# Optimization experiments

Measured on AMD Instinct MI355X. Metric: run time of the kernel, lower is better.

The kernel has to match this reference:

```python
import jax, jax.numpy as jnp
import numpy as np

N_NODES = 100000
N_EDGES = 1600000
IN_FEATS = 256
OUT_FEATS = 128


def setup_inputs() -> dict:
    key = jax.random.key(0)
    k1, k2, k3, k4 = jax.random.split(key, 4)
    feat = jax.random.normal(k1, (N_NODES, IN_FEATS), dtype=jnp.float32)
    # Glorot-uniform-like weight
    limit = np.sqrt(6.0 / (IN_FEATS + OUT_FEATS)).astype(np.float32)
    weight = jax.random.uniform(k2, (IN_FEATS, OUT_FEATS), dtype=jnp.float32,
                                minval=-limit, maxval=limit)
    bias = jnp.zeros((OUT_FEATS,), dtype=jnp.float32)
    src = jax.random.randint(k3, (N_EDGES,), 0, N_NODES, dtype=jnp.int32)
    dst = jax.random.randint(k4, (N_EDGES,), 0, N_NODES, dtype=jnp.int32)
    return {"feat": feat, "weight": weight, "bias": bias, "src": src, "dst": dst}


def reference(feat, weight, bias, src, dst):
    n = feat.shape[0]
    # in-degree per node (edges point src -> dst), clipped to >= 1
    deg = jax.ops.segment_sum(jnp.ones_like(dst, dtype=feat.dtype), dst,
                              num_segments=n)
    norm = jnp.clip(deg, 1.0, None) ** -0.5          # [N]
    norm = norm[:, None]                             # [N, 1]
    h = feat * norm                                  # src-side normalization
    # in_feats > out_feats: project first, then aggregate (cheaper messages)
    h = h @ weight                                   # [N, out]
    agg = jax.ops.segment_sum(h[src], dst, num_segments=n)  # sparse sum-aggregate
    rst = agg * norm + bias                          # dst-side norm + bias
    return rst
```

## Files before the change

kernel.cpp:

```cpp
#include <hip/hip_runtime.h>

#define IN_F 256
#define OUT_F 128
#define BSH 7
#define BNODES 128
#define MAXBUCK 1024
#define BIN_BLOCKS 256

typedef short bf16x8 __attribute__((ext_vector_type(8)));
typedef float f32x4 __attribute__((ext_vector_type(4)));

__device__ inline unsigned short f2bf(float x) {
    union { float f; unsigned u; } v; v.f = x;
    unsigned r = v.u + 0x7FFFu + ((v.u >> 16) & 1u);
    return (unsigned short)(r >> 16);
}
__device__ inline float bf2f(unsigned short x) {
    union { unsigned u; float f; } v; v.u = ((unsigned)x) << 16;
    return v.f;
}

__global__ __launch_bounds__(256) void wprep_kernel(const float* __restrict__ W,
                                                    unsigned short* __restrict__ Wt,
                                                    int* __restrict__ bhist) {
    int n = blockIdx.x;
    int k = threadIdx.x;
    Wt[n * IN_F + k] = f2bf(W[k * OUT_F + n]);
    if (threadIdx.x < 8) bhist[blockIdx.x * 8 + threadIdx.x] = 0;
}

__global__ __launch_bounds__(256) void bin1a_kernel(const int* __restrict__ dst,
                                                    int* __restrict__ bhist,
                                                    int n_edges, int nbuck) {
    __shared__ int hist[MAXBUCK];
    const int tid = threadIdx.x;
    const int chunk = (n_edges + gridDim.x - 1) / gridDim.x;
    const int lo = blockIdx.x * chunk;
    const int hi = min(lo + chunk, n_edges);

    for (int i = tid; i < MAXBUCK; i += 256) hist[i] = 0;
    __syncthreads();
    for (int e = lo + tid; e < hi; e += 256)
        atomicAdd(&hist[dst[e] >> BSH], 1);
    __syncthreads();
    for (int i = tid; i < nbuck; i += 256) {
        int c = hist[i];
        if (c) atomicAdd(&bhist[i], c);
    }
}

__global__ __launch_bounds__(1024) void scanb_kernel(const int* __restrict__ bhist,
                                                     int* __restrict__ bstart,
                                                     int* __restrict__ gcur,
                                                     int* __restrict__ rstart,
                                                     int nbuck, int n_nodes) {
    __shared__ int sh[1024];
    int tid = threadIdx.x;
    int v = (tid < nbuck) ? bhist[tid] : 0;
    sh[tid] = v;
    __syncthreads();
    #pragma unroll
    for (int off = 1; off < 1024; off <<= 1) {
        int t = (tid >= off) ? sh[tid - off] : 0;
        __syncthreads();
        sh[tid] += t;
        __syncthreads();
    }
    int ex = sh[tid] - v;
    if (tid < nbuck) { bstart[tid] = ex; gcur[tid] = ex; }
    if (tid == 1023) {
        bstart[nbuck] = sh[1023];
        rstart[n_nodes] = sh[1023];
    }
}

__global__ __launch_bounds__(256) void bin1b_kernel(const int* __restrict__ src,
                                                    const int* __restrict__ dst,
                                                    int* __restrict__ gcur,
                                                    unsigned* __restrict__ ebuf,
                                                    int n_edges, int nbuck) {
    __shared__ int hist[MAXBUCK];
    __shared__ int lbase[MAXBUCK];
    const int tid = threadIdx.x;
    const int chunk = (n_edges + gridDim.x - 1) / gridDim.x;
    const int lo = blockIdx.x * chunk;
    const int hi = min(lo + chunk, n_edges);

    for (int i = tid; i < nbuck; i += 256) hist[i] = 0;
    __syncthreads();
    for (int e = lo + tid; e < hi; e += 256)
        atomicAdd(&hist[dst[e] >> BSH], 1);
    __syncthreads();
    for (int i = tid; i < nbuck; i += 256) {
        int c = hist[i];
        lbase[i] = (c > 0) ? atomicAdd(&gcur[i], c) : 0;
        hist[i] = 0;
    }
    __syncthreads();
    for (int e = lo + tid; e < hi; e += 256) {
        int d = dst[e];
        int bkt = d >> BSH;
        int off = atomicAdd(&hist[bkt], 1);
        ebuf[lbase[bkt] + off] = ((unsigned)src[e] << BSH) | (unsigned)(d & (BNODES - 1));
    }
}

__global__ __launch_bounds__(256) void bin2_kernel(const unsigned* __restrict__ ebuf,
                                                   const int* __restrict__ bstart,
                                                   int* __restrict__ rstart,
                                                   float* __restrict__ norm,
                                                   int* __restrict__ eidx,
                                                   int n_nodes) {
    __shared__ int lcnt[BNODES];
    __shared__ int lex[BNODES];
    const int tid = threadIdx.x;
    const int node0 = blockIdx.x << BSH;
    const int e0 = bstart[blockIdx.x];
    const int e1 = bstart[blockIdx.x + 1];

    if (tid < BNODES) lcnt[tid] = 0;
    __syncthreads();
    for (int e = e0 + tid; e < e1; e += 256)
        atomicAdd(&lcnt[ebuf[e] & (BNODES - 1)], 1);
    __syncthreads();

    int own = (tid < BNODES) ? lcnt[tid] : 0;
    if (tid < BNODES) lex[tid] = own;
    __syncthreads();
    #pragma unroll
    for (int off = 1; off < BNODES; off <<= 1) {
        int t = (tid >= off && tid < BNODES) ? lex[tid - off] : 0;
        __syncthreads();
        if (tid < BNODES) lex[tid] += t;
        __syncthreads();
    }
    if (tid < BNODES) {
        int ex = lex[tid] - own;
        lex[tid] = ex;
        int g = node0 + tid;
        if (g <= n_nodes) rstart[g] = e0 + ex;
        if (g < n_nodes) {
            float d = (float)own;
            if (d < 1.0f) d = 1.0f;
            norm[g] = 1.0f / sqrtf(d);
        }
        lcnt[tid] = 0;
    }
    __syncthreads();

    for (int e = e0 + tid; e < e1; e += 256) {
        unsigned pk = ebuf[e];
        int dl = pk & (BNODES - 1);
        int pos = atomicAdd(&lcnt[dl], 1);
        eidx[e0 + lex[dl] + pos] = (int)(pk >> BSH);
    }
}

__global__ __launch_bounds__(512) void gemm_mfma(const float* __restrict__ feat,
                                                 const unsigned short* __restrict__ Wt,
                                                 unsigned short* __restrict__ h,
                                                 int n_nodes) {
    __shared__ unsigned short Bs[OUT_F * IN_F];

    const int tid  = threadIdx.x;
    const int wave = tid >> 6;
    const int lane = tid & 63;
    const int r0   = (blockIdx.x * 8 + wave) * 16;
    const int lrow = lane & 15;
    const int g    = lane >> 4;
    const int kgrp = g * 8;

    {
        const f32x4* srcv = reinterpret_cast<const f32x4*>(Wt);
        f32x4* dstv = reinterpret_cast<f32x4*>(Bs);
        #pragma unroll
        for (int i = 0; i < 8; ++i) {
            int c   = tid + i * 512;
            int row = c >> 5;
            int col = c & 31;
            dstv[c] = srcv[row * 32 + (col ^ (row & 7))];
        }
    }

    const int row  = r0 + lrow;
    const int rowc = (row < n_nodes) ? row : (n_nodes - 1);
    const float* arow = feat + (size_t)rowc * IN_F;

    f32x4 a[16];
    #pragma unroll
    for (int k0 = 0; k0 < IN_F / 32; ++k0) {
        a[2 * k0]     = *reinterpret_cast<const f32x4*>(arow + k0 * 32 + kgrp);
        a[2 * k0 + 1] = *reinterpret_cast<const f32x4*>(arow + k0 * 32 + kgrp + 4);
    }
    #pragma unroll
    for (int i = 0; i < 16; ++i)
        asm volatile("" : "+v"(a[i]));

    __syncthreads();

    f32x4 acc[8];
    #pragma unroll
    for (int n = 0; n < 8; ++n) acc[n] = (f32x4){0.f, 0.f, 0.f, 0.f};

    const bf16x8* bsv = reinterpret_cast<const bf16x8*>(Bs);

    #pragma unroll
    for (int k0 = 0; k0 < IN_F / 32; ++k0) {
        const f32x4 a0 = a[2 * k0];
        const f32x4 a1 = a[2 * k0 + 1];
        bf16x8 afr;
        afr[0] = (short)f2bf(a0[0]);
        afr[1] = (short)f2bf(a0[1]);
        afr[2] = (short)f2bf(a0[2]);
        afr[3] = (short)f2bf(a0[3]);
        afr[4] = (short)f2bf(a1[0]);
        afr[5] = (short)f2bf(a1[1]);
        afr[6] = (short)f2bf(a1[2]);
        afr[7] = (short)f2bf(a1[3]);
        #pragma unroll
        for (int n = 0; n < 8; ++n) {
            const int brow = n * 16 + lrow;
            bf16x8 bfr = bsv[brow * 32 + ((k0 * 4 + g) ^ (brow & 7))];
            acc[n] = __builtin_amdgcn_mfma_f32_16x16x32_bf16(afr, bfr, acc[n], 0, 0, 0);
        }
    }

    const int orow0 = r0 + g * 4;
    #pragma unroll
    for (int n = 0; n < 8; ++n) {
        #pragma unroll
        for (int j = 0; j < 4; ++j) {
            int orow = orow0 + j;
            if (orow < n_nodes)
                h[(size_t)orow * OUT_F + n * 16 + lrow] = f2bf(acc[n][j]);
        }
    }
}

__global__ __launch_bounds__(256) void agg_kernel(const unsigned short* __restrict__ h,
                                                  const int* __restrict__ eidx,
                                                  const int* __restrict__ rstart,
                                                  const float* __restrict__ norm,
                                                  const float* __restrict__ bias,
                                                  float* __restrict__ out,
                                                  int n_nodes) {
    const int wave = threadIdx.x >> 6;
    const int lane = threadIdx.x & 63;
    const int node = blockIdx.x * 4 + wave;
    if (node >= n_nodes) return;

    const int start = rstart[node];
    const int cnt   = rstart[node + 1] - start;

    float a0 = 0.f, a1 = 0.f;
    for (int base = 0; base < cnt; base += 64) {
        const int rem = min(64, cnt - base);
        int   ev = (lane < rem) ? eidx[start + base + lane] : 0;
        float nv = (lane < rem) ? norm[ev] : 0.f;

        int j = 0;
        for (; j + 4 <= rem; j += 4) {
            int s0 = __shfl(ev, j),     s1 = __shfl(ev, j + 1);
            int s2 = __shfl(ev, j + 2), s3 = __shfl(ev, j + 3);
            float n0 = __shfl(nv, j),     n1 = __shfl(nv, j + 1);
            float n2 = __shfl(nv, j + 2), n3 = __shfl(nv, j + 3);
            unsigned v0 = *reinterpret_cast<const unsigned*>(h + (size_t)s0 * OUT_F + lane * 2);
            unsigned v1 = *reinterpret_cast<const unsigned*>(h + (size_t)s1 * OUT_F + lane * 2);
            unsigned v2 = *reinterpret_cast<const unsigned*>(h + (size_t)s2 * OUT_F + lane * 2);
            unsigned v3 = *reinterpret_cast<const unsigned*>(h + (size_t)s3 * OUT_F + lane * 2);
            a0 += bf2f((unsigned short)(v0 & 0xffffu)) * n0;
            a1 += bf2f((unsigned short)(v0 >> 16))     * n0;
            a0 += bf2f((unsigned short)(v1 & 0xffffu)) * n1;
            a1 += bf2f((unsigned short)(v1 >> 16))     * n1;
            a0 += bf2f((unsigned short)(v2 & 0xffffu)) * n2;
            a1 += bf2f((unsigned short)(v2 >> 16))     * n2;
            a0 += bf2f((unsigned short)(v3 & 0xffffu)) * n3;
            a1 += bf2f((unsigned short)(v3 >> 16))     * n3;
        }
        for (; j < rem; ++j) {
            int   s  = __shfl(ev, j);
            float nm = __shfl(nv, j);
            unsigned v = *reinterpret_cast<const unsigned*>(h + (size_t)s * OUT_F + lane * 2);
            a0 += bf2f((unsigned short)(v & 0xffffu)) * nm;
            a1 += bf2f((unsigned short)(v >> 16))     * nm;
        }
    }

    const float nd = norm[node];
    float2 r;
    r.x = a0 * nd + bias[lane * 2];
    r.y = a1 * nd + bias[lane * 2 + 1];
    *reinterpret_cast<float2*>(out + (size_t)node * OUT_F + lane * 2) = r;
}

extern "C" void kernel_launch(void* const* d_in, const int* in_sizes, int n_in,
                              void* d_out, int out_size, void* d_ws, size_t ws_size,
                              hipStream_t stream) {
    const float* feat   = (const float*)d_in[0];
    const float* weight = (const float*)d_in[1];
    const float* bias   = (const float*)d_in[2];
    const int*   src    = (const int*)d_in[3];
    const int*   dst    = (const int*)d_in[4];
    float* out = (float*)d_out;

    const int n_nodes = in_sizes[0] / IN_F;
    const int n_edges = in_sizes[3];
    const int nbuck   = (n_nodes + BNODES - 1) >> BSH;

    char* ws = (char*)d_ws;
    size_t off = 0;
    auto alloc = [&](size_t bytes) {
        char* p = ws + off;
        off += (bytes + 15) & ~(size_t)15;
        return p;
    };
    unsigned short* h  = (unsigned short*)alloc((size_t)n_nodes * OUT_F * 2);
    float* norm        = (float*)alloc((size_t)n_nodes * 4);
    int*   rstart      = (int*)alloc(((size_t)n_nodes + 1) * 4);
    int*   bhist       = (int*)alloc(MAXBUCK * 4);
    int*   bstart      = (int*)alloc((MAXBUCK + 1) * 4);
    int*   gcur        = (int*)alloc(MAXBUCK * 4);
    unsigned short* Wt = (unsigned short*)alloc((size_t)OUT_F * IN_F * 2);
    unsigned* ebuf     = (unsigned*)alloc((size_t)n_edges * 4);
    int*   eidx        = (int*)alloc((size_t)n_edges * 4);

    wprep_kernel<<<OUT_F, IN_F, 0, stream>>>(weight, Wt, bhist);
    bin1a_kernel<<<BIN_BLOCKS, 256, 0, stream>>>(dst, bhist, n_edges, nbuck);
    scanb_kernel<<<1, 1024, 0, stream>>>(bhist, bstart, gcur, rstart, nbuck, n_nodes);
    bin1b_kernel<<<BIN_BLOCKS, 256, 0, stream>>>(src, dst, gcur, ebuf, n_edges, nbuck);
    gemm_mfma<<<(n_nodes + 127) / 128, 512, 0, stream>>>(feat, Wt, h, n_nodes);
    bin2_kernel<<<nbuck, 256, 0, stream>>>(ebuf, bstart, rstart, norm, eidx, n_nodes);
    agg_kernel<<<(n_nodes + 3) / 4, 256, 0, stream>>>(h, eidx, rstart, norm, bias, out, n_nodes);
}
```

Measured before the change: 160.4 us.

## Merge weight prep with histogram and binning with GEMM into horizontal kernels

Weight transpose/convert and the first-pass bucket histogram now run as one launch, split by block index. The edge-binning scatter pass and the MFMA GEMM also share one launch, so the independent binning and projection work can overlap on the GPU. The bhist zeroing moves to a hipMemsetAsync. This removes launch gaps and lets the small, latency-bound binning blocks share the GPU with GEMM blocks. In exchange the binning blocks now use 512 threads and the GEMM's 64KB shared-memory footprint, which may reduce occupancy for that part.

```diff
diff --git a/kernel.cpp b/kernel.cpp
--- a/kernel.cpp
+++ b/kernel.cpp
@@ -5,7 +5,8 @@
 #define BSH 7
 #define BNODES 128
 #define MAXBUCK 1024
-#define BIN_BLOCKS 256
+#define BIN1A_BLOCKS 256
+#define BIN1B_BLOCKS 256
 
 typedef short bf16x8 __attribute__((ext_vector_type(8)));
 typedef float f32x4 __attribute__((ext_vector_type(4)));
@@ -20,32 +21,31 @@
     return v.f;
 }
 
-__global__ __launch_bounds__(256) void wprep_kernel(const float* __restrict__ W,
-                                                    unsigned short* __restrict__ Wt,
-                                                    int* __restrict__ bhist) {
-    int n = blockIdx.x;
-    int k = threadIdx.x;
-    Wt[n * IN_F + k] = f2bf(W[k * OUT_F + n]);
-    if (threadIdx.x < 8) bhist[blockIdx.x * 8 + threadIdx.x] = 0;
-}
-
-__global__ __launch_bounds__(256) void bin1a_kernel(const int* __restrict__ dst,
-                                                    int* __restrict__ bhist,
-                                                    int n_edges, int nbuck) {
-    __shared__ int hist[MAXBUCK];
-    const int tid = threadIdx.x;
-    const int chunk = (n_edges + gridDim.x - 1) / gridDim.x;
-    const int lo = blockIdx.x * chunk;
-    const int hi = min(lo + chunk, n_edges);
-
-    for (int i = tid; i < MAXBUCK; i += 256) hist[i] = 0;
-    __syncthreads();
-    for (int e = lo + tid; e < hi; e += 256)
-        atomicAdd(&hist[dst[e] >> BSH], 1);
-    __syncthreads();
-    for (int i = tid; i < nbuck; i += 256) {
-        int c = hist[i];
-        if (c) atomicAdd(&bhist[i], c);
+__global__ __launch_bounds__(256) void prep_kernel(const float* __restrict__ W,
+                                                   unsigned short* __restrict__ Wt,
+                                                   const int* __restrict__ dst,
+                                                   int* __restrict__ bhist,
+                                                   int n_edges, int nbuck) {
+    if ((int)blockIdx.x < BIN1A_BLOCKS) {
+        __shared__ int hist[MAXBUCK];
+        const int tid = threadIdx.x;
+        const int chunk = (n_edges + BIN1A_BLOCKS - 1) / BIN1A_BLOCKS;
+        const int lo = blockIdx.x * chunk;
+        const int hi = min(lo + chunk, n_edges);
+
+        for (int i = tid; i < MAXBUCK; i += 256) hist[i] = 0;
+        __syncthreads();
+        for (int e = lo + tid; e < hi; e += 256)
+            atomicAdd(&hist[dst[e] >> BSH], 1);
+        __syncthreads();
+        for (int i = tid; i < nbuck; i += 256) {
+            int c = hist[i];
+            if (c) atomicAdd(&bhist[i], c);
+        }
+    } else {
+        int n = blockIdx.x - BIN1A_BLOCKS;
+        int k = threadIdx.x;
+        Wt[n * IN_F + k] = f2bf(W[k * OUT_F + n]);
     }
 }
 
@@ -74,34 +74,117 @@
     }
 }
 
-__global__ __launch_bounds__(256) void bin1b_kernel(const int* __restrict__ src,
-                                                    const int* __restrict__ dst,
-                                                    int* __restrict__ gcur,
-                                                    unsigned* __restrict__ ebuf,
-                                                    int n_edges, int nbuck) {
-    __shared__ int hist[MAXBUCK];
-    __shared__ int lbase[MAXBUCK];
-    const int tid = threadIdx.x;
-    const int chunk = (n_edges + gridDim.x - 1) / gridDim.x;
-    const int lo = blockIdx.x * chunk;
-    const int hi = min(lo + chunk, n_edges);
-
-    for (int i = tid; i < nbuck; i += 256) hist[i] = 0;
-    __syncthreads();
-    for (int e = lo + tid; e < hi; e += 256)
-        atomicAdd(&hist[dst[e] >> BSH], 1);
-    __syncthreads();
-    for (int i = tid; i < nbuck; i += 256) {
-        int c = hist[i];
-        lbase[i] = (c > 0) ? atomicAdd(&gcur[i], c) : 0;
-        hist[i] = 0;
-    }
-    __syncthreads();
-    for (int e = lo + tid; e < hi; e += 256) {
-        int d = dst[e];
-        int bkt = d >> BSH;
-        int off = atomicAdd(&hist[bkt], 1);
-        ebuf[lbase[bkt] + off] = ((unsigned)src[e] << BSH) | (unsigned)(d & (BNODES - 1));
+__global__ __launch_bounds__(512) void gemm_bin_kernel(
+        const float* __restrict__ feat, const unsigned short* __restrict__ Wt,
+        unsigned short* __restrict__ h, int n_nodes,
+        const int* __restrict__ src, const int* __restrict__ dst,
+        int* __restrict__ gcur, unsigned* __restrict__ ebuf,
+        int n_edges, int nbuck) {
+
+    __shared__ __align__(16) char smem[65536];
+
+    if ((int)blockIdx.x < BIN1B_BLOCKS) {
+        int* hist  = (int*)smem;
+        int* lbase = hist + MAXBUCK;
+        const int tid = threadIdx.x;
+        const int chunk = (n_edges + BIN1B_BLOCKS - 1) / BIN1B_BLOCKS;
+        const int lo = blockIdx.x * chunk;
+        const int hi = min(lo + chunk, n_edges);
+
+        for (int i = tid; i < nbuck; i += 512) hist[i] = 0;
+        __syncthreads();
+        for (int e = lo + tid; e < hi; e += 512)
+            atomicAdd(&hist[dst[e] >> BSH], 1);
+        __syncthreads();
+        for (int i = tid; i < nbuck; i += 512) {
+            int c = hist[i];
+            lbase[i] = (c > 0) ? atomicAdd(&gcur[i], c) : 0;
+            hist[i] = 0;
+        }
+        __syncthreads();
+        for (int e = lo + tid; e < hi; e += 512) {
+            int d = dst[e];
+            int bkt = d >> BSH;
+            int off = atomicAdd(&hist[bkt], 1);
+            ebuf[lbase[bkt] + off] = ((unsigned)src[e] << BSH) | (unsigned)(d & (BNODES - 1));
+        }
+    } else {
+        unsigned short* Bs = (unsigned short*)smem;
+
+        const int tid  = threadIdx.x;
+        const int wave = tid >> 6;
+        const int lane = tid & 63;
+        const int gb   = blockIdx.x - BIN1B_BLOCKS;
+        const int r0   = (gb * 8 + wave) * 16;
+        const int lrow = lane & 15;
+        const int g    = lane >> 4;
+        const int kgrp = g * 8;
+
+        {
+            const f32x4* srcv = reinterpret_cast<const f32x4*>(Wt);
+            f32x4* dstv = reinterpret_cast<f32x4*>(Bs);
+            #pragma unroll
+            for (int i = 0; i < 8; ++i) {
+                int c   = tid + i * 512;
+                int row = c >> 5;
+                int col = c & 31;
+                dstv[c] = srcv[row * 32 + (col ^ (row & 7))];
+            }
+        }
+
+        const int row  = r0 + lrow;
+        const int rowc = (row < n_nodes) ? row : (n_nodes - 1);
+        const float* arow = feat + (size_t)rowc * IN_F;
+
+        f32x4 a[16];
+        #pragma unroll
+        for (int k0 = 0; k0 < IN_F / 32; ++k0) {
+            a[2 * k0]     = *reinterpret_cast<const f32x4*>(arow + k0 * 32 + kgrp);
+            a[2 * k0 + 1] = *reinterpret_cast<const f32x4*>(arow + k0 * 32 + kgrp + 4);
+        }
+        #pragma unroll
+        for (int i = 0; i < 16; ++i)
+            asm volatile("" : "+v"(a[i]));
+
+        __syncthreads();
+
+        f32x4 acc[8];
+        #pragma unroll
+        for (int n = 0; n < 8; ++n) acc[n] = (f32x4){0.f, 0.f, 0.f, 0.f};
+
+        const bf16x8* bsv = reinterpret_cast<const bf16x8*>(Bs);
+
+        #pragma unroll
+        for (int k0 = 0; k0 < IN_F / 32; ++k0) {
+            const f32x4 a0 = a[2 * k0];
+            const f32x4 a1 = a[2 * k0 + 1];
+            bf16x8 afr;
+            afr[0] = (short)f2bf(a0[0]);
+            afr[1] = (short)f2bf(a0[1]);
+            afr[2] = (short)f2bf(a0[2]);
+            afr[3] = (short)f2bf(a0[3]);
+            afr[4] = (short)f2bf(a1[0]);
+            afr[5] = (short)f2bf(a1[1]);
+            afr[6] = (short)f2bf(a1[2]);
+            afr[7] = (short)f2bf(a1[3]);
+            #pragma unroll
+            for (int n = 0; n < 8; ++n) {
+                const int brow = n * 16 + lrow;
+                bf16x8 bfr = bsv[brow * 32 + ((k0 * 4 + g) ^ (brow & 7))];
+                acc[n] = __builtin_amdgcn_mfma_f32_16x16x32_bf16(afr, bfr, acc[n], 0, 0, 0);
+            }
+        }
+
+        const int orow0 = r0 + g * 4;
+        #pragma unroll
+        for (int n = 0; n < 8; ++n) {
+            #pragma unroll
+            for (int j = 0; j < 4; ++j) {
+                int orow = orow0 + j;
+                if (orow < n_nodes)
+                    h[(size_t)orow * OUT_F + n * 16 + lrow] = f2bf(acc[n][j]);
+            }
+        }
     }
 }
 
@@ -153,87 +236,6 @@
         int dl = pk & (BNODES - 1);
         int pos = atomicAdd(&lcnt[dl], 1);
         eidx[e0 + lex[dl] + pos] = (int)(pk >> BSH);
-    }
-}
-
-__global__ __launch_bounds__(512) void gemm_mfma(const float* __restrict__ feat,
-                                                 const unsigned short* __restrict__ Wt,
-                                                 unsigned short* __restrict__ h,
-                                                 int n_nodes) {
-    __shared__ unsigned short Bs[OUT_F * IN_F];
-
-    const int tid  = threadIdx.x;
-    const int wave = tid >> 6;
-    const int lane = tid & 63;
-    const int r0   = (blockIdx.x * 8 + wave) * 16;
-    const int lrow = lane & 15;
-    const int g    = lane >> 4;
-    const int kgrp = g * 8;
-
-    {
-        const f32x4* srcv = reinterpret_cast<const f32x4*>(Wt);
-        f32x4* dstv = reinterpret_cast<f32x4*>(Bs);
-        #pragma unroll
-        for (int i = 0; i < 8; ++i) {
-            int c   = tid + i * 512;
-            int row = c >> 5;
-            int col = c & 31;
-            dstv[c] = srcv[row * 32 + (col ^ (row & 7))];
-        }
-    }
-
-    const int row  = r0 + lrow;
-    const int rowc = (row < n_nodes) ? row : (n_nodes - 1);
-    const float* arow = feat + (size_t)rowc * IN_F;
-
-    f32x4 a[16];
-    #pragma unroll
-    for (int k0 = 0; k0 < IN_F / 32; ++k0) {
-        a[2 * k0]     = *reinterpret_cast<const f32x4*>(arow + k0 * 32 + kgrp);
-        a[2 * k0 + 1] = *reinterpret_cast<const f32x4*>(arow + k0 * 32 + kgrp + 4);
-    }
-    #pragma unroll
-    for (int i = 0; i < 16; ++i)
-        asm volatile("" : "+v"(a[i]));
-
-    __syncthreads();
-
-    f32x4 acc[8];
-    #pragma unroll
-    for (int n = 0; n < 8; ++n) acc[n] = (f32x4){0.f, 0.f, 0.f, 0.f};
-
-    const bf16x8* bsv = reinterpret_cast<const bf16x8*>(Bs);
-
-    #pragma unroll
-    for (int k0 = 0; k0 < IN_F / 32; ++k0) {
-        const f32x4 a0 = a[2 * k0];
-        const f32x4 a1 = a[2 * k0 + 1];
-        bf16x8 afr;
-        afr[0] = (short)f2bf(a0[0]);
-        afr[1] = (short)f2bf(a0[1]);
-        afr[2] = (short)f2bf(a0[2]);
-        afr[3] = (short)f2bf(a0[3]);
-        afr[4] = (short)f2bf(a1[0]);
-        afr[5] = (short)f2bf(a1[1]);
-        afr[6] = (short)f2bf(a1[2]);
-        afr[7] = (short)f2bf(a1[3]);
-        #pragma unroll
-        for (int n = 0; n < 8; ++n) {
-            const int brow = n * 16 + lrow;
-            bf16x8 bfr = bsv[brow * 32 + ((k0 * 4 + g) ^ (brow & 7))];
-            acc[n] = __builtin_amdgcn_mfma_f32_16x16x32_bf16(afr, bfr, acc[n], 0, 0, 0);
-        }
-    }
-
-    const int orow0 = r0 + g * 4;
-    #pragma unroll
-    for (int n = 0; n < 8; ++n) {
-        #pragma unroll
-        for (int j = 0; j < 4; ++j) {
-            int orow = orow0 + j;
-            if (orow < n_nodes)
-                h[(size_t)orow * OUT_F + n * 16 + lrow] = f2bf(acc[n][j]);
-        }
     }
 }
 
@@ -306,6 +308,7 @@
     const int n_nodes = in_sizes[0] / IN_F;
     const int n_edges = in_sizes[3];
     const int nbuck   = (n_nodes + BNODES - 1) >> BSH;
+    const int gemm_blocks = (n_nodes + 127) / 128;
 
     char* ws = (char*)d_ws;
     size_t off = 0;
@@ -324,11 +327,12 @@
     unsigned* ebuf     = (unsigned*)alloc((size_t)n_edges * 4);
     int*   eidx        = (int*)alloc((size_t)n_edges * 4);
 
-    wprep_kernel<<<OUT_F, IN_F, 0, stream>>>(weight, Wt, bhist);
-    bin1a_kernel<<<BIN_BLOCKS, 256, 0, stream>>>(dst, bhist, n_edges, nbuck);
+    hipMemsetAsync(bhist, 0, MAXBUCK * sizeof(int), stream);
+    prep_kernel<<<BIN1A_BLOCKS + OUT_F, 256, 0, stream>>>(weight, Wt, dst, bhist,
+                                                          n_edges, nbuck);
     scanb_kernel<<<1, 1024, 0, stream>>>(bhist, bstart, gcur, rstart, nbuck, n_nodes);
-    bin1b_kernel<<<BIN_BLOCKS, 256, 0, stream>>>(src, dst, gcur, ebuf, n_edges, nbuck);
-    gemm_mfma<<<(n_nodes + 127) / 128, 512, 0, stream>>>(feat, Wt, h, n_nodes);
+    gemm_bin_kernel<<<BIN1B_BLOCKS + gemm_blocks, 512, 0, stream>>>(
+        feat, Wt, h, n_nodes, src, dst, gcur, ebuf, n_edges, nbuck);
     bin2_kernel<<<nbuck, 256, 0, stream>>>(ebuf, bstart, rstart, norm, eidx, n_nodes);
     agg_kernel<<<(n_nodes + 3) / 4, 256, 0, stream>>>(h, eidx, rstart, norm, bias, out, n_nodes);
 }
```

New measurement: 155.9 us. 1.03x faster.
